# Kernel tuning notes

Hardware: AMD Instinct MI355X
Metric: run time of the kernel (lower is better)

The kernel has to match this reference:

```python
import jax, jax.numpy as jnp
import numpy as np

H, W, D, C = 32, 16, 16, 4
NUM_ITERS = 2
THETA_GAMMA = 3.0   # spatial (position-only) kernel bandwidth
THETA_ALPHA = 8.0   # bilateral position bandwidth
THETA_BETA = 0.5    # bilateral color bandwidth


def _attn(feats, q):
    # Gaussian-kernel attention: softmax_j(-0.5 * ||f_i - f_j||^2) @ q
    # feats: [N, F], q: [N, C] -> [N, C]
    sq = jnp.sum(feats * feats, axis=-1)
    logits = feats @ feats.T - 0.5 * (sq[:, None] + sq[None, :])  # [N, N]
    return jax.nn.softmax(logits, axis=-1) @ q


def setup_inputs() -> dict:
    key = jax.random.key(0)
    k1, k2 = jax.random.split(key)
    unaries = jax.random.normal(k1, (1, H, W, D, C), dtype=jnp.float32)
    rgb = jax.random.normal(k2, (1, H, W, D, 3), dtype=jnp.float32)
    eye = jnp.eye(C, dtype=jnp.float32)
    return {
        "unaries": unaries,
        "rgb": rgb,
        "spatial_ker_weights": eye,          # _diagonal_initializer
        "bilateral_ker_weights": eye,        # _diagonal_initializer
        "compatibility_matrix": -eye,        # _potts_model_initializer
    }


def reference(unaries, rgb, spatial_ker_weights, bilateral_ker_weights, compatibility_matrix):
    N = H * W * D
    # positions start at 1 as in tf.range(1, h+1)
    grids = jnp.meshgrid(jnp.arange(1, H + 1), jnp.arange(1, W + 1), jnp.arange(1, D + 1), indexing='ij')
    pos = jnp.stack(grids, axis=-1).astype(jnp.float32).reshape(N, 3)
    rgb_flat = rgb.reshape(N, 3)
    spatial_feats = pos / THETA_GAMMA                                             # [N, 3]
    bilateral_feats = jnp.concatenate([pos / THETA_ALPHA, rgb_flat / THETA_BETA], axis=-1)  # [N, 6]

    u = unaries.reshape(N, C)
    q = u
    for _ in range(NUM_ITERS):
        sm = jax.nn.softmax(q, axis=-1)                         # [N, C]
        spatial_out = _attn(spatial_feats, sm)                  # [N, C]
        bilateral_out = _attn(bilateral_feats, sm)              # [N, C]
        # message_passing = SK @ spatial + BK @ bilateral (class-space matmul)
        message = spatial_out @ spatial_ker_weights.T + bilateral_out @ bilateral_ker_weights.T
        pairwise = message @ compatibility_matrix.T             # [N, C]
        q = u + pairwise
    return q.reshape(unaries.shape)
```

## Files before the change

### kernel.cpp

```cpp
#include <hip/hip_runtime.h>


#define HH 32
#define WW 16
#define DDD 16
#define NN (HH * WW * DDD)
#define KS 128
#define JC (NN / KS)
#define CONVB 32
#define GB 2048
#define L2E 1.4426950408889634f
#define C18 (L2E / 18.0f)
#define SQL2E 1.2011224087864498f
#define SB (SQL2E / 8.0f)
#define SC (SQL2E / 0.5f)

#if __has_builtin(__builtin_amdgcn_exp2f)
#define EXP2(x) __builtin_amdgcn_exp2f(x)
#else
#define EXP2(x) exp2f(x)
#endif

__global__ __launch_bounds__(256) void prep(
    const float* __restrict__ u, const float* __restrict__ rgb,
    float* __restrict__ feats, float* __restrict__ sm0)
{
    int i = blockIdx.x * 256 + threadIdx.x;
    int h = i >> 8, r = i & 255, w = r >> 4, d = r & 15;
    float fh = (float)(h + 1) * SB;
    float fw = (float)(w + 1) * SB;
    float fd = (float)(d + 1) * SB;
    float c0 = rgb[3 * i + 0] * SC;
    float c1 = rgb[3 * i + 1] * SC;
    float c2 = rgb[3 * i + 2] * SC;
    float nn = -0.5f * (fh * fh + fw * fw + fd * fd + c0 * c0 + c1 * c1 + c2 * c2);
    ((float4*)feats)[2 * i + 0] = make_float4(fh, fw, fd, c0);
    ((float4*)feats)[2 * i + 1] = make_float4(c1, c2, nn, 0.0f);

    float4 q = ((const float4*)u)[i];
    float m = fmaxf(fmaxf(q.x, q.y), fmaxf(q.z, q.w));
    float e0 = EXP2((q.x - m) * L2E), e1 = EXP2((q.y - m) * L2E);
    float e2 = EXP2((q.z - m) * L2E), e3 = EXP2((q.w - m) * L2E);
    float rs = 1.0f / (e0 + e1 + e2 + e3);
    ((float4*)sm0)[i] = make_float4(e0 * rs, e1 * rs, e2 * rs, e3 * rs);
}

__global__ __launch_bounds__(256, 8) void fused(
    const float* __restrict__ sm,
    const float* __restrict__ feats,
    float* __restrict__ part,
    float* __restrict__ tmp)
{
    __shared__ float lds[2048];
    int tid = threadIdx.x;

    if (blockIdx.x >= CONVB) {
        int b = blockIdx.x - CONVB;
        int ib = b >> 7;
        int kc = b & (KS - 1);
        int i0 = ib * 512 + tid;
        int i1 = i0 + 256;
        int j0 = kc * JC;

        const float4* f4 = (const float4*)feats;
        const float4* s4 = (const float4*)sm;

        float4* lrec = (float4*)lds;
        if (tid < 128) {
            float4 v = f4[2 * j0 + tid];
            lrec[(tid >> 1) * 3 + (tid & 1)] = v;
        } else if (tid < 192) {
            int jj = tid - 128;
            lrec[jj * 3 + 2] = s4[j0 + jj];
        }

        float4 A0 = f4[2 * i0], A1 = f4[2 * i0 + 1];
        float4 B0 = f4[2 * i1], B1 = f4[2 * i1 + 1];
        float dfh = B0.x - A0.x;
        float dc0 = B0.w - A0.w, dc1 = B1.x - A1.x, dc2 = B1.y - A1.y;
        float dn  = B1.z - A1.z;
        __syncthreads();

        float a0 = 0, a1 = 0, a2 = 0, a3 = 0;
        float b0 = 0, b1 = 0, b2 = 0, b3 = 0;

        #pragma unroll 4
        for (int jj = 0; jj < JC; ++jj) {
            float4 r0 = lrec[jj * 3 + 0];
            float4 r1 = lrec[jj * 3 + 1];
            float4 s  = lrec[jj * 3 + 2];
            float g0 = A1.z + r1.z;
            g0 = fmaf(A0.x, r0.x, g0);
            g0 = fmaf(A0.y, r0.y, g0);
            g0 = fmaf(A0.z, r0.z, g0);
            g0 = fmaf(A0.w, r0.w, g0);
            g0 = fmaf(A1.x, r1.x, g0);
            g0 = fmaf(A1.y, r1.y, g0);
            float g1 = fmaf(dfh, r0.x, g0 + dn);
            g1 = fmaf(dc0, r0.w, g1);
            g1 = fmaf(dc1, r1.x, g1);
            g1 = fmaf(dc2, r1.y, g1);
            float w0 = EXP2(g0);
            float w1 = EXP2(g1);
            a0 = fmaf(w0, s.x, a0); a1 = fmaf(w0, s.y, a1);
            a2 = fmaf(w0, s.z, a2); a3 = fmaf(w0, s.w, a3);
            b0 = fmaf(w1, s.x, b0); b1 = fmaf(w1, s.y, b1);
            b2 = fmaf(w1, s.z, b2); b3 = fmaf(w1, s.w, b3);
        }

        float4* p = (float4*)(part + (size_t)kc * (NN * 4));
        p[i0] = make_float4(a0, a1, a2, a3);
        p[i1] = make_float4(b0, b1, b2, b3);
    } else {
        int h = blockIdx.x;
        int s = tid;
        int i = h * 256 + s;

        float* A = lds;
        float* B = lds + 1024;
        *((float4*)(A + 4 * s)) = ((const float4*)sm)[i];
        __syncthreads();

        int w = s >> 4, d = s & 15;
        float t0 = 0, t1 = 0, t2 = 0, t3 = 0;
        #pragma unroll
        for (int dp = 0; dp < DDD; ++dp) {
            float dd = (float)(d - dp);
            float k = EXP2(-dd * dd * C18);
            const float4 v = *((const float4*)(A + 4 * (w * 16 + dp)));
            t0 = fmaf(k, v.x, t0); t1 = fmaf(k, v.y, t1);
            t2 = fmaf(k, v.z, t2); t3 = fmaf(k, v.w, t3);
        }
        *((float4*)(B + 4 * s)) = make_float4(t0, t1, t2, t3);
        __syncthreads();

        float u0 = 0, u1 = 0, u2 = 0, u3 = 0;
        #pragma unroll
        for (int wp = 0; wp < WW; ++wp) {
            float dw = (float)(w - wp);
            float k = EXP2(-dw * dw * C18);
            const float4 v = *((const float4*)(B + 4 * (wp * 16 + d)));
            u0 = fmaf(k, v.x, u0); u1 = fmaf(k, v.y, u1);
            u2 = fmaf(k, v.z, u2); u3 = fmaf(k, v.w, u3);
        }
        *((float4*)(tmp + 4 * i)) = make_float4(u0, u1, u2, u3);
    }
}

__global__ __launch_bounds__(256) void reduce_finish(
    const float* __restrict__ part,
    const float* __restrict__ tmp,
    const float* __restrict__ u,
    const float* __restrict__ sk, const float* __restrict__ bk,
    const float* __restrict__ cm,
    float* __restrict__ qout,
    float* __restrict__ smout)
{
    int tid = threadIdx.x;
    int q = tid >> 6;
    int lane = tid & 63;
    int idx = blockIdx.x * 64 + lane;

    float bl = 0.0f;
    #pragma unroll
    for (int k = 0; k < KS / 4; ++k)
        bl += part[(size_t)(q * (KS / 4) + k) * (NN * 4) + idx];

    int i = idx >> 2;
    int h = i >> 8;
    int scid = idx & 1023;
    float sp = 0.0f;
    #pragma unroll
    for (int k = 0; k < 8; ++k) {
        int hp = q * 8 + k;
        float dh = (float)(h - hp);
        float kk = EXP2(-dh * dh * C18);
        sp = fmaf(kk, tmp[hp * 1024 + scid], sp);
    }

    __shared__ float Lb[4][64];
    __shared__ float Ls[4][64];
    Lb[q][lane] = bl;
    Ls[q][lane] = sp;
    __syncthreads();

    if (tid < 16) {
        float b4[4], s4[4];
        #pragma unroll
        for (int c = 0; c < 4; ++c) {
            int l = tid * 4 + c;
            b4[c] = Lb[0][l] + Lb[1][l] + Lb[2][l] + Lb[3][l];
            s4[c] = Ls[0][l] + Ls[1][l] + Ls[2][l] + Ls[3][l];
        }
        float rb = 1.0f / (b4[0] + b4[1] + b4[2] + b4[3]);
        float rs = 1.0f / (s4[0] + s4[1] + s4[2] + s4[3]);
        float bo[4], so[4];
        #pragma unroll
        for (int c = 0; c < 4; ++c) { bo[c] = b4[c] * rb; so[c] = s4[c] * rs; }
        float msg[4];
        #pragma unroll
        for (int c = 0; c < 4; ++c) {
            float m = 0.0f;
            #pragma unroll
            for (int d = 0; d < 4; ++d)
                m += sk[c * 4 + d] * so[d] + bk[c * 4 + d] * bo[d];
            msg[c] = m;
        }
        int ig = blockIdx.x * 16 + tid;
        float qv[4];
        #pragma unroll
        for (int c = 0; c < 4; ++c) {
            float pw = 0.0f;
            #pragma unroll
            for (int d = 0; d < 4; ++d) pw += cm[c * 4 + d] * msg[d];
            qv[c] = u[4 * ig + c] + pw;
        }
        *((float4*)(qout + 4 * ig)) = make_float4(qv[0], qv[1], qv[2], qv[3]);

        float mm = fmaxf(fmaxf(qv[0], qv[1]), fmaxf(qv[2], qv[3]));
        float e0 = EXP2((qv[0] - mm) * L2E), e1 = EXP2((qv[1] - mm) * L2E);
        float e2 = EXP2((qv[2] - mm) * L2E), e3 = EXP2((qv[3] - mm) * L2E);
        float er = 1.0f / (e0 + e1 + e2 + e3);
        *((float4*)(smout + 4 * ig)) = make_float4(e0 * er, e1 * er, e2 * er, e3 * er);
    }
}

extern "C" void kernel_launch(void* const* d_in, const int* in_sizes, int n_in,
                              void* d_out, int out_size, void* d_ws, size_t ws_size,
                              hipStream_t stream)
{
    const float* u   = (const float*)d_in[0];
    const float* rgb = (const float*)d_in[1];
    const float* sk  = (const float*)d_in[2];
    const float* bk  = (const float*)d_in[3];
    const float* cm  = (const float*)d_in[4];
    float* out = (float*)d_out;

    float* part   = (float*)d_ws;
    float* feats  = part  + (size_t)KS * NN * 4;
    float* tmpP   = feats + (size_t)NN * 8;
    float* smA    = tmpP  + (size_t)NN * 4;
    float* smB    = smA   + (size_t)NN * 4;
    float* qbuf   = smB   + (size_t)NN * 4;
    float* smDead = qbuf  + (size_t)NN * 4;

    dim3 blk(256);
    dim3 gP(NN / 256);
    dim3 gF(CONVB + GB);
    dim3 gR(NN * 4 / 64);

    prep<<<gP, blk, 0, stream>>>(u, rgb, feats, smA);
    fused<<<gF, blk, 0, stream>>>(smA, feats, part, tmpP);
    reduce_finish<<<gR, blk, 0, stream>>>(part, tmpP, u, sk, bk, cm, qbuf, smB);
    fused<<<gF, blk, 0, stream>>>(smB, feats, part, tmpP);
    reduce_finish<<<gR, blk, 0, stream>>>(part, tmpP, u, sk, bk, cm, out, smDead);
}
```

Measured before the change: 68.36 us.

## Register-block eight query rows per thread and double the key split count

```diff
diff --git a/kernel.cpp b/kernel.cpp
--- a/kernel.cpp
+++ b/kernel.cpp
@@ -5,10 +5,12 @@
 #define WW 16
 #define DDD 16
 #define NN (HH * WW * DDD)
-#define KS 128
+#define KS 256
 #define JC (NN / KS)
 #define CONVB 32
-#define GB 2048
+#define RROWS 8
+#define ITILES (NN / (256 * RROWS))
+#define GB (ITILES * KS)
 #define L2E 1.4426950408889634f
 #define C18 (L2E / 18.0f)
 #define SQL2E 1.2011224087864498f
@@ -45,7 +47,7 @@
     ((float4*)sm0)[i] = make_float4(e0 * rs, e1 * rs, e2 * rs, e3 * rs);
 }
 
-__global__ __launch_bounds__(256, 8) void fused(
+__global__ __launch_bounds__(256, 4) void fused(
     const float* __restrict__ sm,
     const float* __restrict__ feats,
     float* __restrict__ part,
@@ -56,61 +58,78 @@
 
     if (blockIdx.x >= CONVB) {
         int b = blockIdx.x - CONVB;
-        int ib = b >> 7;
+        int ib = b >> 8;
         int kc = b & (KS - 1);
-        int i0 = ib * 512 + tid;
-        int i1 = i0 + 256;
+        int i0 = ib * 2048 + tid;
         int j0 = kc * JC;
 
         const float4* f4 = (const float4*)feats;
         const float4* s4 = (const float4*)sm;
 
         float4* lrec = (float4*)lds;
-        if (tid < 128) {
+        if (tid < 2 * JC) {
             float4 v = f4[2 * j0 + tid];
             lrec[(tid >> 1) * 3 + (tid & 1)] = v;
-        } else if (tid < 192) {
-            int jj = tid - 128;
+        } else if (tid < 3 * JC) {
+            int jj = tid - 2 * JC;
             lrec[jj * 3 + 2] = s4[j0 + jj];
         }
 
-        float4 A0 = f4[2 * i0], A1 = f4[2 * i0 + 1];
-        float4 B0 = f4[2 * i1], B1 = f4[2 * i1 + 1];
-        float dfh = B0.x - A0.x;
-        float dc0 = B0.w - A0.w, dc1 = B1.x - A1.x, dc2 = B1.y - A1.y;
-        float dn  = B1.z - A1.z;
+        float4 P0 = f4[2 * i0];
+        float4 P1 = f4[2 * i0 + 1];
+        float dc0[RROWS - 1], dc1[RROWS - 1], dc2[RROWS - 1], dnn[RROWS - 1];
+        #pragma unroll
+        for (int k = 1; k < RROWS; ++k) {
+            float4 Q0 = f4[2 * i0 + 512 * k];
+            float4 Q1 = f4[2 * i0 + 512 * k + 1];
+            dc0[k - 1] = Q0.w - P0.w;
+            dc1[k - 1] = Q1.x - P1.x;
+            dc2[k - 1] = Q1.y - P1.y;
+            dnn[k - 1] = Q1.z - P1.z;
+        }
         __syncthreads();
 
-        float a0 = 0, a1 = 0, a2 = 0, a3 = 0;
-        float b0 = 0, b1 = 0, b2 = 0, b3 = 0;
-
-        #pragma unroll 4
+        float acc[RROWS][4];
+        #pragma unroll
+        for (int k = 0; k < RROWS; ++k)
+            #pragma unroll
+            for (int c = 0; c < 4; ++c) acc[k][c] = 0.0f;
+
+        #pragma unroll 2
         for (int jj = 0; jj < JC; ++jj) {
             float4 r0 = lrec[jj * 3 + 0];
             float4 r1 = lrec[jj * 3 + 1];
             float4 s  = lrec[jj * 3 + 2];
-            float g0 = A1.z + r1.z;
-            g0 = fmaf(A0.x, r0.x, g0);
-            g0 = fmaf(A0.y, r0.y, g0);
-            g0 = fmaf(A0.z, r0.z, g0);
-            g0 = fmaf(A0.w, r0.w, g0);
-            g0 = fmaf(A1.x, r1.x, g0);
-            g0 = fmaf(A1.y, r1.y, g0);
-            float g1 = fmaf(dfh, r0.x, g0 + dn);
-            g1 = fmaf(dc0, r0.w, g1);
-            g1 = fmaf(dc1, r1.x, g1);
-            g1 = fmaf(dc2, r1.y, g1);
+            float g0 = P1.z + r1.z;
+            g0 = fmaf(P0.x, r0.x, g0);
+            g0 = fmaf(P0.y, r0.y, g0);
+            g0 = fmaf(P0.z, r0.z, g0);
+            g0 = fmaf(P0.w, r0.w, g0);
+            g0 = fmaf(P1.x, r1.x, g0);
+            g0 = fmaf(P1.y, r1.y, g0);
             float w0 = EXP2(g0);
-            float w1 = EXP2(g1);
-            a0 = fmaf(w0, s.x, a0); a1 = fmaf(w0, s.y, a1);
-            a2 = fmaf(w0, s.z, a2); a3 = fmaf(w0, s.w, a3);
-            b0 = fmaf(w1, s.x, b0); b1 = fmaf(w1, s.y, b1);
-            b2 = fmaf(w1, s.z, b2); b3 = fmaf(w1, s.w, b3);
+            acc[0][0] = fmaf(w0, s.x, acc[0][0]);
+            acc[0][1] = fmaf(w0, s.y, acc[0][1]);
+            acc[0][2] = fmaf(w0, s.z, acc[0][2]);
+            acc[0][3] = fmaf(w0, s.w, acc[0][3]);
+            #pragma unroll
+            for (int k = 1; k < RROWS; ++k) {
+                float g = fmaf((float)k * SB, r0.x, g0 + dnn[k - 1]);
+                g = fmaf(dc0[k - 1], r0.w, g);
+                g = fmaf(dc1[k - 1], r1.x, g);
+                g = fmaf(dc2[k - 1], r1.y, g);
+                float wk = EXP2(g);
+                acc[k][0] = fmaf(wk, s.x, acc[k][0]);
+                acc[k][1] = fmaf(wk, s.y, acc[k][1]);
+                acc[k][2] = fmaf(wk, s.z, acc[k][2]);
+                acc[k][3] = fmaf(wk, s.w, acc[k][3]);
+            }
         }
 
         float4* p = (float4*)(part + (size_t)kc * (NN * 4));
-        p[i0] = make_float4(a0, a1, a2, a3);
-        p[i1] = make_float4(b0, b1, b2, b3);
+        #pragma unroll
+        for (int k = 0; k < RROWS; ++k)
+            p[i0 + 256 * k] = make_float4(acc[k][0], acc[k][1], acc[k][2], acc[k][3]);
     } else {
         int h = blockIdx.x;
         int s = tid;
@@ -162,7 +181,7 @@
     int idx = blockIdx.x * 64 + lane;
 
     float bl = 0.0f;
-    #pragma unroll
+    #pragma unroll 8
     for (int k = 0; k < KS / 4; ++k)
         bl += part[(size_t)(q * (KS / 4) + k) * (NN * 4) + idx];
 
```

After: 78.97 us. 1.16x slower.

## Compute bilateral attention with bf16 MFMA using hi/lo split features

Applied to the files above, without the earlier changes.

```diff
diff --git a/kernel.cpp b/kernel.cpp
--- a/kernel.cpp
+++ b/kernel.cpp
@@ -5,10 +5,11 @@
 #define WW 16
 #define DDD 16
 #define NN (HH * WW * DDD)
-#define KS 128
-#define JC (NN / KS)
+#define KS 16
+#define JCH (NN / KS)
 #define CONVB 32
-#define GB 2048
+#define ITILB (NN / 64)
+#define GB2 (ITILB * KS)
 #define L2E 1.4426950408889634f
 #define C18 (L2E / 18.0f)
 #define SQL2E 1.2011224087864498f
@@ -21,98 +22,126 @@
 #define EXP2(x) exp2f(x)
 #endif
 
+typedef __attribute__((ext_vector_type(8))) short bf16x8;
+typedef __attribute__((ext_vector_type(4))) float f32x4;
+#define MFMA16 __builtin_amdgcn_mfma_f32_16x16x32_bf16
+
+__device__ __forceinline__ unsigned short f2bf(float x) {
+    unsigned int u = __float_as_uint(x);
+    return (unsigned short)((u + 0x7FFFu + ((u >> 16) & 1u)) >> 16);
+}
+__device__ __forceinline__ float bf2f(unsigned short b) {
+    return __uint_as_float(((unsigned int)b) << 16);
+}
+__device__ __forceinline__ unsigned int pk(unsigned short a, unsigned short b) {
+    return (unsigned int)a | ((unsigned int)b << 16);
+}
+
 __global__ __launch_bounds__(256) void prep(
     const float* __restrict__ u, const float* __restrict__ rgb,
-    float* __restrict__ feats, float* __restrict__ sm0)
+    unsigned short* __restrict__ fq, unsigned short* __restrict__ fk,
+    float* __restrict__ sm0, unsigned short* __restrict__ smT0)
 {
     int i = blockIdx.x * 256 + threadIdx.x;
     int h = i >> 8, r = i & 255, w = r >> 4, d = r & 15;
-    float fh = (float)(h + 1) * SB;
-    float fw = (float)(w + 1) * SB;
-    float fd = (float)(d + 1) * SB;
-    float c0 = rgb[3 * i + 0] * SC;
-    float c1 = rgb[3 * i + 1] * SC;
-    float c2 = rgb[3 * i + 2] * SC;
-    float nn = -0.5f * (fh * fh + fw * fw + fd * fd + c0 * c0 + c1 * c1 + c2 * c2);
-    ((float4*)feats)[2 * i + 0] = make_float4(fh, fw, fd, c0);
-    ((float4*)feats)[2 * i + 1] = make_float4(c1, c2, nn, 0.0f);
+    float f[6];
+    f[0] = (float)(h + 1) * SB;
+    f[1] = (float)(w + 1) * SB;
+    f[2] = (float)(d + 1) * SB;
+    f[3] = rgb[3 * i + 0] * SC;
+    f[4] = rgb[3 * i + 1] * SC;
+    f[5] = rgb[3 * i + 2] * SC;
+    float nh = -0.5f * (f[0]*f[0] + f[1]*f[1] + f[2]*f[2] +
+                        f[3]*f[3] + f[4]*f[4] + f[5]*f[5]);
+    unsigned short hi[7], lo[7];
+    #pragma unroll
+    for (int k = 0; k < 6; ++k) {
+        hi[k] = f2bf(f[k]);
+        lo[k] = f2bf(f[k] - bf2f(hi[k]));
+    }
+    hi[6] = f2bf(nh);
+    lo[6] = f2bf(nh - bf2f(hi[6]));
+    const unsigned short one = 0x3F80;
+
+    uint4* q4 = (uint4*)(fq + (size_t)i * 32);
+    uint4* k4 = (uint4*)(fk + (size_t)i * 32);
+    q4[0] = make_uint4(pk(hi[0],hi[1]), pk(hi[2],hi[3]), pk(hi[4],hi[5]), pk(hi[6],one));
+    q4[1] = make_uint4(pk(lo[0],lo[1]), pk(lo[2],lo[3]), pk(lo[4],lo[5]), pk(lo[6],0));
+    q4[2] = make_uint4(pk(hi[0],hi[1]), pk(hi[2],hi[3]), pk(hi[4],hi[5]), pk(0,one));
+    q4[3] = make_uint4(0, 0, 0, 0);
+    k4[0] = make_uint4(pk(hi[0],hi[1]), pk(hi[2],hi[3]), pk(hi[4],hi[5]), pk(one,hi[6]));
+    k4[1] = make_uint4(pk(hi[0],hi[1]), pk(hi[2],hi[3]), pk(hi[4],hi[5]), pk(one,0));
+    k4[2] = make_uint4(pk(lo[0],lo[1]), pk(lo[2],lo[3]), pk(lo[4],lo[5]), pk(0,lo[6]));
+    k4[3] = make_uint4(0, 0, 0, 0);
 
     float4 q = ((const float4*)u)[i];
     float m = fmaxf(fmaxf(q.x, q.y), fmaxf(q.z, q.w));
     float e0 = EXP2((q.x - m) * L2E), e1 = EXP2((q.y - m) * L2E);
     float e2 = EXP2((q.z - m) * L2E), e3 = EXP2((q.w - m) * L2E);
     float rs = 1.0f / (e0 + e1 + e2 + e3);
-    ((float4*)sm0)[i] = make_float4(e0 * rs, e1 * rs, e2 * rs, e3 * rs);
+    float s0 = e0 * rs, s1 = e1 * rs, s2 = e2 * rs, s3 = e3 * rs;
+    ((float4*)sm0)[i] = make_float4(s0, s1, s2, s3);
+    smT0[0 * NN + i] = f2bf(s0);
+    smT0[1 * NN + i] = f2bf(s1);
+    smT0[2 * NN + i] = f2bf(s2);
+    smT0[3 * NN + i] = f2bf(s3);
 }
 
 __global__ __launch_bounds__(256, 8) void fused(
     const float* __restrict__ sm,
-    const float* __restrict__ feats,
+    const unsigned short* __restrict__ smT,
+    const unsigned short* __restrict__ fq,
+    const unsigned short* __restrict__ fk,
     float* __restrict__ part,
     float* __restrict__ tmp)
 {
     __shared__ float lds[2048];
     int tid = threadIdx.x;
 
-    if (blockIdx.x >= CONVB) {
-        int b = blockIdx.x - CONVB;
-        int ib = b >> 7;
+    if (blockIdx.x < GB2) {
+        int b = blockIdx.x;
+        int ibk = b >> 4;
         int kc = b & (KS - 1);
-        int i0 = ib * 512 + tid;
-        int i1 = i0 + 256;
-        int j0 = kc * JC;
-
-        const float4* f4 = (const float4*)feats;
-        const float4* s4 = (const float4*)sm;
-
-        float4* lrec = (float4*)lds;
-        if (tid < 128) {
-            float4 v = f4[2 * j0 + tid];
-            lrec[(tid >> 1) * 3 + (tid & 1)] = v;
-        } else if (tid < 192) {
-            int jj = tid - 128;
-            lrec[jj * 3 + 2] = s4[j0 + jj];
-        }
-
-        float4 A0 = f4[2 * i0], A1 = f4[2 * i0 + 1];
-        float4 B0 = f4[2 * i1], B1 = f4[2 * i1 + 1];
-        float dfh = B0.x - A0.x;
-        float dc0 = B0.w - A0.w, dc1 = B1.x - A1.x, dc2 = B1.y - A1.y;
-        float dn  = B1.z - A1.z;
-        __syncthreads();
-
-        float a0 = 0, a1 = 0, a2 = 0, a3 = 0;
-        float b0 = 0, b1 = 0, b2 = 0, b3 = 0;
-
-        #pragma unroll 4
-        for (int jj = 0; jj < JC; ++jj) {
-            float4 r0 = lrec[jj * 3 + 0];
-            float4 r1 = lrec[jj * 3 + 1];
-            float4 s  = lrec[jj * 3 + 2];
-            float g0 = A1.z + r1.z;
-            g0 = fmaf(A0.x, r0.x, g0);
-            g0 = fmaf(A0.y, r0.y, g0);
-            g0 = fmaf(A0.z, r0.z, g0);
-            g0 = fmaf(A0.w, r0.w, g0);
-            g0 = fmaf(A1.x, r1.x, g0);
-            g0 = fmaf(A1.y, r1.y, g0);
-            float g1 = fmaf(dfh, r0.x, g0 + dn);
-            g1 = fmaf(dc0, r0.w, g1);
-            g1 = fmaf(dc1, r1.x, g1);
-            g1 = fmaf(dc2, r1.y, g1);
-            float w0 = EXP2(g0);
-            float w1 = EXP2(g1);
-            a0 = fmaf(w0, s.x, a0); a1 = fmaf(w0, s.y, a1);
-            a2 = fmaf(w0, s.z, a2); a3 = fmaf(w0, s.w, a3);
-            b0 = fmaf(w1, s.x, b0); b1 = fmaf(w1, s.y, b1);
-            b2 = fmaf(w1, s.z, b2); b3 = fmaf(w1, s.w, b3);
-        }
-
-        float4* p = (float4*)(part + (size_t)kc * (NN * 4));
-        p[i0] = make_float4(a0, a1, a2, a3);
-        p[i1] = make_float4(b0, b1, b2, b3);
+        int wv = tid >> 6, lane = tid & 63;
+        int lm = lane & 15, lg = lane >> 4;
+        int i0 = ibk * 64 + wv * 16;
+        int j0 = kc * JCH;
+
+        const bf16x8* FQ = (const bf16x8*)fq;
+        const bf16x8* FK = (const bf16x8*)fk;
+        bf16x8 Bf = FK[(size_t)(i0 + lm) * 4 + lg];
+        const unsigned short* smc = smT + (size_t)(lm & 3) * NN;
+
+        unsigned int* P = (unsigned int*)lds + wv * 320;
+        f32x4 acc = {0.f, 0.f, 0.f, 0.f};
+        const f32x4 zro = {0.f, 0.f, 0.f, 0.f};
+
+        #pragma unroll 2
+        for (int s = 0; s < JCH / 32; ++s) {
+            int js = j0 + s * 32;
+            bf16x8 A0 = FQ[(size_t)(js + lm) * 4 + lg];
+            bf16x8 A1 = FQ[(size_t)(js + 16 + lm) * 4 + lg];
+            f32x4 S0 = MFMA16(A0, Bf, zro, 0, 0, 0);
+            f32x4 S1 = MFMA16(A1, Bf, zro, 0, 0, 0);
+            uint2 w0, w1;
+            w0.x = pk(f2bf(EXP2(S0[0])), f2bf(EXP2(S0[1])));
+            w0.y = pk(f2bf(EXP2(S0[2])), f2bf(EXP2(S0[3])));
+            w1.x = pk(f2bf(EXP2(S1[0])), f2bf(EXP2(S1[1])));
+            w1.y = pk(f2bf(EXP2(S1[2])), f2bf(EXP2(S1[3])));
+            *(uint2*)(P + lm * 20 + 2 * lg)     = w0;
+            *(uint2*)(P + lm * 20 + 2 * lg + 8) = w1;
+            bf16x8 Pf = *(const bf16x8*)(P + lm * 20 + 4 * lg);
+            bf16x8 Sf = *(const bf16x8*)(smc + js + 8 * lg);
+            acc = MFMA16(Pf, Sf, acc, 0, 0, 0);
+        }
+        if (lm < 4) {
+            float* pp = part + (size_t)kc * (NN * 4);
+            #pragma unroll
+            for (int r = 0; r < 4; ++r)
+                pp[(size_t)(i0 + 4 * lg + r) * 4 + lm] = acc[r];
+        }
     } else {
-        int h = blockIdx.x;
+        int h = blockIdx.x - GB2;
         int s = tid;
         int i = h * 256 + s;
 
@@ -154,7 +183,8 @@
     const float* __restrict__ sk, const float* __restrict__ bk,
     const float* __restrict__ cm,
     float* __restrict__ qout,
-    float* __restrict__ smout)
+    float* __restrict__ smout,
+    unsigned short* __restrict__ smTout)
 {
     int tid = threadIdx.x;
     int q = tid >> 6;
@@ -221,7 +251,12 @@
         float e0 = EXP2((qv[0] - mm) * L2E), e1 = EXP2((qv[1] - mm) * L2E);
         float e2 = EXP2((qv[2] - mm) * L2E), e3 = EXP2((qv[3] - mm) * L2E);
         float er = 1.0f / (e0 + e1 + e2 + e3);
-        *((float4*)(smout + 4 * ig)) = make_float4(e0 * er, e1 * er, e2 * er, e3 * er);
+        float sv0 = e0 * er, sv1 = e1 * er, sv2 = e2 * er, sv3 = e3 * er;
+        *((float4*)(smout + 4 * ig)) = make_float4(sv0, sv1, sv2, sv3);
+        smTout[0 * NN + ig] = f2bf(sv0);
+        smTout[1 * NN + ig] = f2bf(sv1);
+        smTout[2 * NN + ig] = f2bf(sv2);
+        smTout[3 * NN + ig] = f2bf(sv3);
     }
 }
 
@@ -236,22 +271,24 @@
     const float* cm  = (const float*)d_in[4];
     float* out = (float*)d_out;
 
-    float* part   = (float*)d_ws;
-    float* feats  = part  + (size_t)KS * NN * 4;
-    float* tmpP   = feats + (size_t)NN * 8;
-    float* smA    = tmpP  + (size_t)NN * 4;
-    float* smB    = smA   + (size_t)NN * 4;
-    float* qbuf   = smB   + (size_t)NN * 4;
-    float* smDead = qbuf  + (size_t)NN * 4;
+    float* part = (float*)d_ws;
+    float* tmpP = part + (size_t)KS * NN * 4;
+    float* smA  = tmpP + (size_t)NN * 4;
+    float* smB  = smA  + (size_t)NN * 4;
+    float* qbuf = smB  + (size_t)NN * 4;
+    unsigned short* fq   = (unsigned short*)(qbuf + (size_t)NN * 4);
+    unsigned short* fk   = fq + (size_t)NN * 32;
+    unsigned short* smTA = fk + (size_t)NN * 32;
+    unsigned short* smTB = smTA + (size_t)NN * 4;
 
     dim3 blk(256);
     dim3 gP(NN / 256);
-    dim3 gF(CONVB + GB);
+    dim3 gF(GB2 + CONVB);
     dim3 gR(NN * 4 / 64);
 
-    prep<<<gP, blk, 0, stream>>>(u, rgb, feats, smA);
-    fused<<<gF, blk, 0, stream>>>(smA, feats, part, tmpP);
-    reduce_finish<<<gR, blk, 0, stream>>>(part, tmpP, u, sk, bk, cm, qbuf, smB);
-    fused<<<gF, blk, 0, stream>>>(smB, feats, part, tmpP);
-    reduce_finish<<<gR, blk, 0, stream>>>(part, tmpP, u, sk, bk, cm, out, smDead);
-}
+    prep<<<gP, blk, 0, stream>>>(u, rgb, fq, fk, smA, smTA);
+    fused<<<gF, blk, 0, stream>>>(smA, smTA, fq, fk, part, tmpP);
+    reduce_finish<<<gR, blk, 0, stream>>>(part, tmpP, u, sk, bk, cm, qbuf, smB, smTB);
+    fused<<<gF, blk, 0, stream>>>(smB, smTB, fq, fk, part, tmpP);
+    reduce_finish<<<gR, blk, 0, stream>>>(part, tmpP, u, sk, bk, cm, out, smA, smTA);
+}
```

Measured after the change: 76.82 us. +12.4%, slower.

## Factor bilateral logits into position and color terms, tile four rows per thread

Applied to the files above, without the earlier changes.

```diff
diff --git a/kernel.cpp b/kernel.cpp
--- a/kernel.cpp
+++ b/kernel.cpp
@@ -8,7 +8,8 @@
 #define KS 128
 #define JC (NN / KS)
 #define CONVB 32
-#define GB 2048
+#define ITIL 8
+#define GB (ITIL * KS)
 #define L2E 1.4426950408889634f
 #define C18 (L2E / 18.0f)
 #define SQL2E 1.2011224087864498f
@@ -21,9 +22,23 @@
 #define EXP2(x) exp2f(x)
 #endif
 
+__device__ __forceinline__ unsigned short f2bf(float x) {
+    unsigned int u = __float_as_uint(x);
+    return (unsigned short)((u + 0x7FFFu + ((u >> 16) & 1u)) >> 16);
+}
+__device__ __forceinline__ unsigned int pk2(unsigned short a, unsigned short b) {
+    return (unsigned int)a | ((unsigned int)b << 16);
+}
+__device__ __forceinline__ float bfLO(unsigned int u) {
+    return __uint_as_float(u << 16);
+}
+__device__ __forceinline__ float bfHI(unsigned int u) {
+    return __uint_as_float(u & 0xFFFF0000u);
+}
+
 __global__ __launch_bounds__(256) void prep(
     const float* __restrict__ u, const float* __restrict__ rgb,
-    float* __restrict__ feats, float* __restrict__ sm0)
+    float4* __restrict__ cpk, uint2* __restrict__ smb)
 {
     int i = blockIdx.x * 256 + threadIdx.x;
     int h = i >> 8, r = i & 255, w = r >> 4, d = r & 15;
@@ -33,21 +48,22 @@
     float c0 = rgb[3 * i + 0] * SC;
     float c1 = rgb[3 * i + 1] * SC;
     float c2 = rgb[3 * i + 2] * SC;
-    float nn = -0.5f * (fh * fh + fw * fw + fd * fd + c0 * c0 + c1 * c1 + c2 * c2);
-    ((float4*)feats)[2 * i + 0] = make_float4(fh, fw, fd, c0);
-    ((float4*)feats)[2 * i + 1] = make_float4(c1, c2, nn, 0.0f);
+    float nj = -0.5f * (fh * fh + fw * fw + fd * fd +
+                        c0 * c0 + c1 * c1 + c2 * c2);
+    cpk[i] = make_float4(c0, c1, c2, nj);
 
     float4 q = ((const float4*)u)[i];
     float m = fmaxf(fmaxf(q.x, q.y), fmaxf(q.z, q.w));
     float e0 = EXP2((q.x - m) * L2E), e1 = EXP2((q.y - m) * L2E);
     float e2 = EXP2((q.z - m) * L2E), e3 = EXP2((q.w - m) * L2E);
     float rs = 1.0f / (e0 + e1 + e2 + e3);
-    ((float4*)sm0)[i] = make_float4(e0 * rs, e1 * rs, e2 * rs, e3 * rs);
-}
-
-__global__ __launch_bounds__(256, 8) void fused(
-    const float* __restrict__ sm,
-    const float* __restrict__ feats,
+    smb[i] = make_uint2(pk2(f2bf(e0 * rs), f2bf(e1 * rs)),
+                        pk2(f2bf(e2 * rs), f2bf(e3 * rs)));
+}
+
+__global__ __launch_bounds__(256, 4) void fused(
+    const uint2* __restrict__ smb,
+    const float4* __restrict__ cpk,
     float* __restrict__ part,
     float* __restrict__ tmp)
 {
@@ -58,67 +74,76 @@
         int b = blockIdx.x - CONVB;
         int ib = b >> 7;
         int kc = b & (KS - 1);
-        int i0 = ib * 512 + tid;
-        int i1 = i0 + 256;
+        int i0 = ib * 1024 + tid;
         int j0 = kc * JC;
 
-        const float4* f4 = (const float4*)feats;
-        const float4* s4 = (const float4*)sm;
-
-        float4* lrec = (float4*)lds;
-        if (tid < 128) {
-            float4 v = f4[2 * j0 + tid];
-            lrec[(tid >> 1) * 3 + (tid & 1)] = v;
-        } else if (tid < 192) {
-            int jj = tid - 128;
-            lrec[jj * 3 + 2] = s4[j0 + jj];
-        }
-
-        float4 A0 = f4[2 * i0], A1 = f4[2 * i0 + 1];
-        float4 B0 = f4[2 * i1], B1 = f4[2 * i1 + 1];
-        float dfh = B0.x - A0.x;
-        float dc0 = B0.w - A0.w, dc1 = B1.x - A1.x, dc2 = B1.y - A1.y;
-        float dn  = B1.z - A1.z;
+        float4* recs4 = (float4*)lds;
+        uint2*  recs2 = (uint2*)(lds + 256);
+
+        if (tid < JC) {
+            recs4[tid] = cpk[j0 + tid];
+            recs2[tid] = smb[j0 + tid];
+        }
+
+        float fw = (float)((tid >> 4) + 1) * SB;
+        float fd = (float)((tid & 15) + 1) * SB;
+        float gh = (float)((j0 >> 8) + 1) * SB;
+        float4 cp[4];
+        float  K[4];
+        #pragma unroll
+        for (int r = 0; r < 4; ++r) {
+            cp[r] = cpk[i0 + 256 * r];
+            float fh = (float)(ib * 4 + r + 1) * SB;
+            K[r] = cp[r].w + fh * gh;
+        }
+        float acc[4][4];
+        #pragma unroll
+        for (int r = 0; r < 4; ++r)
+            #pragma unroll
+            for (int c = 0; c < 4; ++c) acc[r][c] = 0.0f;
+
         __syncthreads();
 
-        float a0 = 0, a1 = 0, a2 = 0, a3 = 0;
-        float b0 = 0, b1 = 0, b2 = 0, b3 = 0;
-
-        #pragma unroll 4
-        for (int jj = 0; jj < JC; ++jj) {
-            float4 r0 = lrec[jj * 3 + 0];
-            float4 r1 = lrec[jj * 3 + 1];
-            float4 s  = lrec[jj * 3 + 2];
-            float g0 = A1.z + r1.z;
-            g0 = fmaf(A0.x, r0.x, g0);
-            g0 = fmaf(A0.y, r0.y, g0);
-            g0 = fmaf(A0.z, r0.z, g0);
-            g0 = fmaf(A0.w, r0.w, g0);
-            g0 = fmaf(A1.x, r1.x, g0);
-            g0 = fmaf(A1.y, r1.y, g0);
-            float g1 = fmaf(dfh, r0.x, g0 + dn);
-            g1 = fmaf(dc0, r0.w, g1);
-            g1 = fmaf(dc1, r1.x, g1);
-            g1 = fmaf(dc2, r1.y, g1);
-            float w0 = EXP2(g0);
-            float w1 = EXP2(g1);
-            a0 = fmaf(w0, s.x, a0); a1 = fmaf(w0, s.y, a1);
-            a2 = fmaf(w0, s.z, a2); a3 = fmaf(w0, s.w, a3);
-            b0 = fmaf(w1, s.x, b0); b1 = fmaf(w1, s.y, b1);
-            b2 = fmaf(w1, s.z, b2); b3 = fmaf(w1, s.w, b3);
-        }
-
-        float4* p = (float4*)(part + (size_t)kc * (NN * 4));
-        p[i0] = make_float4(a0, a1, a2, a3);
-        p[i1] = make_float4(b0, b1, b2, b3);
+        for (int jw = 0; jw < 4; ++jw) {
+            float gw = (float)(((kc & 3) * 4 + jw) + 1) * SB;
+            #pragma unroll 8
+            for (int jd = 0; jd < 16; ++jd) {
+                int jj = jw * 16 + jd;
+                float gd = (float)(jd + 1) * SB;
+                float4 r4 = recs4[jj];
+                uint2  r2 = recs2[jj];
+                float gpos = fmaf(fw, gw, fmaf(fd, gd, r4.w));
+                float sm0 = bfLO(r2.x), sm1 = bfHI(r2.x);
+                float sm2 = bfLO(r2.y), sm3 = bfHI(r2.y);
+                #pragma unroll
+                for (int r = 0; r < 4; ++r) {
+                    float g = fmaf(cp[r].x, r4.x, K[r]);
+                    g = fmaf(cp[r].y, r4.y, g);
+                    g = fmaf(cp[r].z, r4.z, g);
+                    g += gpos;
+                    float wgt = EXP2(g);
+                    acc[r][0] = fmaf(wgt, sm0, acc[r][0]);
+                    acc[r][1] = fmaf(wgt, sm1, acc[r][1]);
+                    acc[r][2] = fmaf(wgt, sm2, acc[r][2]);
+                    acc[r][3] = fmaf(wgt, sm3, acc[r][3]);
+                }
+            }
+        }
+
+        float4* pp = (float4*)(part + (size_t)kc * (NN * 4));
+        #pragma unroll
+        for (int r = 0; r < 4; ++r)
+            pp[i0 + 256 * r] = make_float4(acc[r][0], acc[r][1], acc[r][2], acc[r][3]);
     } else {
         int h = blockIdx.x;
         int s = tid;
         int i = h * 256 + s;
 
+        uint2 sb = smb[i];
         float* A = lds;
         float* B = lds + 1024;
-        *((float4*)(A + 4 * s)) = ((const float4*)sm)[i];
+        *((float4*)(A + 4 * s)) = make_float4(bfLO(sb.x), bfHI(sb.x),
+                                              bfLO(sb.y), bfHI(sb.y));
         __syncthreads();
 
         int w = s >> 4, d = s & 15;
@@ -154,7 +179,7 @@
     const float* __restrict__ sk, const float* __restrict__ bk,
     const float* __restrict__ cm,
     float* __restrict__ qout,
-    float* __restrict__ smout)
+    uint2* __restrict__ smbOut)
 {
     int tid = threadIdx.x;
     int q = tid >> 6;
@@ -162,7 +187,7 @@
     int idx = blockIdx.x * 64 + lane;
 
     float bl = 0.0f;
-    #pragma unroll
+    #pragma unroll 8
     for (int k = 0; k < KS / 4; ++k)
         bl += part[(size_t)(q * (KS / 4) + k) * (NN * 4) + idx];
 
@@ -221,7 +246,8 @@
         float e0 = EXP2((qv[0] - mm) * L2E), e1 = EXP2((qv[1] - mm) * L2E);
         float e2 = EXP2((qv[2] - mm) * L2E), e3 = EXP2((qv[3] - mm) * L2E);
         float er = 1.0f / (e0 + e1 + e2 + e3);
-        *((float4*)(smout + 4 * ig)) = make_float4(e0 * er, e1 * er, e2 * er, e3 * er);
+        smbOut[ig] = make_uint2(pk2(f2bf(e0 * er), f2bf(e1 * er)),
+                                pk2(f2bf(e2 * er), f2bf(e3 * er)));
     }
 }
 
@@ -236,22 +262,22 @@
     const float* cm  = (const float*)d_in[4];
     float* out = (float*)d_out;
 
-    float* part   = (float*)d_ws;
-    float* feats  = part  + (size_t)KS * NN * 4;
-    float* tmpP   = feats + (size_t)NN * 8;
-    float* smA    = tmpP  + (size_t)NN * 4;
-    float* smB    = smA   + (size_t)NN * 4;
-    float* qbuf   = smB   + (size_t)NN * 4;
-    float* smDead = qbuf  + (size_t)NN * 4;
+    float* part  = (float*)d_ws;
+    float* tmpP  = part + (size_t)KS * NN * 4;
+    float* qbuf  = tmpP + (size_t)NN * 4;
+    float4* cpk  = (float4*)(qbuf + (size_t)NN * 4);
+    uint2* smbA  = (uint2*)(cpk + NN);
+    uint2* smbB  = smbA + NN;
+    uint2* smbD  = smbB + NN;
 
     dim3 blk(256);
     dim3 gP(NN / 256);
     dim3 gF(CONVB + GB);
     dim3 gR(NN * 4 / 64);
 
-    prep<<<gP, blk, 0, stream>>>(u, rgb, feats, smA);
-    fused<<<gF, blk, 0, stream>>>(smA, feats, part, tmpP);
-    reduce_finish<<<gR, blk, 0, stream>>>(part, tmpP, u, sk, bk, cm, qbuf, smB);
-    fused<<<gF, blk, 0, stream>>>(smB, feats, part, tmpP);
-    reduce_finish<<<gR, blk, 0, stream>>>(part, tmpP, u, sk, bk, cm, out, smDead);
-}
+    prep<<<gP, blk, 0, stream>>>(u, rgb, cpk, smbA);
+    fused<<<gF, blk, 0, stream>>>(smbA, cpk, part, tmpP);
+    reduce_finish<<<gR, blk, 0, stream>>>(part, tmpP, u, sk, bk, cm, qbuf, smbB);
+    fused<<<gF, blk, 0, stream>>>(smbB, cpk, part, tmpP);
+    reduce_finish<<<gR, blk, 0, stream>>>(part, tmpP, u, sk, bk, cm, out, smbD);
+}
```

New measurement: 69.45 us. Within noise of the previous version (+1.6%).
